# Optimization experiments

Measured on AMD Instinct MI355X. Metric: run time of the kernel, lower is better.

Reference implementation:

```python
import jax, jax.numpy as jnp
import numpy as np

D = 512
SCALE = 1.0 / np.sqrt(D).astype(np.float32)


def setup_inputs() -> dict:
    key = jax.random.key(0)
    ks = jax.random.split(key, 6)
    B, S = 8, 2048
    x = jax.random.normal(ks[0], (B, S, D), dtype=jnp.float32)
    bias = jax.random.normal(ks[1], (1,), dtype=jnp.float32)
    key_padding_mask = jax.random.randint(ks[2], (B, S), 0, 2).astype(jnp.bool_)
    # nn.Linear weights, stored as [out, in]; y = x @ W.T
    Wq = jax.random.normal(ks[3], (D, D), dtype=jnp.float32) * (1.0 / np.sqrt(D))
    Wk = jax.random.normal(ks[4], (D, D), dtype=jnp.float32) * (1.0 / np.sqrt(D))
    Wv = jax.random.normal(ks[5], (D, D), dtype=jnp.float32) * (1.0 / np.sqrt(D))
    return {"x": x, "bias": bias, "key_padding_mask": key_padding_mask,
            "Wq": Wq, "Wk": Wk, "Wv": Wv}


def reference(x, bias, key_padding_mask, Wq, Wk, Wv):
    # Projections (Linear without bias): [B,S,D] @ [D,D]^T
    Q = jnp.einsum('bsd,ed->bse', x, Wq)
    K = jnp.einsum('bsd,ed->bse', x, Wk)
    V = jnp.einsum('bsd,ed->bse', x, Wv)
    # Scaled scores with additive scalar bias: [B,S,S]
    scores = jnp.einsum('bqd,bkd->bqk', Q, K) * SCALE + bias
    # Key padding mask: mask keys (last dim) with -inf
    scores = jnp.where(key_padding_mask[:, None, :], -jnp.inf, scores)
    attn = jax.nn.softmax(scores, axis=-1)
    attn = jnp.nan_to_num(attn, nan=0.0)  # fully-masked rows -> 0
    # Dropout is inference no-op
    return jnp.einsum('bqk,bkd->bqd', attn, V)
```

## Files before the change

kernel.cpp:

```cpp
#include <hip/hip_runtime.h>

typedef short bf16x8 __attribute__((ext_vector_type(8)));
typedef float f32x4 __attribute__((ext_vector_type(4)));
typedef float f32x16 __attribute__((ext_vector_type(16)));
typedef ushort u16x8 __attribute__((ext_vector_type(8)));

__device__ __forceinline__ ushort f2bf(float f) {
    union { float f; unsigned u; } v; v.f = f;
    unsigned r = (v.u + 0x7fffu + ((v.u >> 16) & 1u)) >> 16;
    return (ushort)r;
}
__device__ __forceinline__ float bf2f(ushort u) {
    union { unsigned u; float f; } v; v.u = ((unsigned)u) << 16;
    return v.f;
}
__device__ __forceinline__ void async_copy16(void* lds, const void* g) {
    __builtin_amdgcn_global_load_lds(
        (const __attribute__((address_space(1))) unsigned*)g,
        (__attribute__((address_space(3))) unsigned*)lds, 16, 0, 0);
}

__global__ __launch_bounds__(256)
void prep_kernel(const float* __restrict__ x, const float* __restrict__ Wq,
                 const float* __restrict__ Wk, const float* __restrict__ Wv,
                 const int* __restrict__ mask,
                 ushort* __restrict__ xb, ushort* __restrict__ wqT,
                 ushort* __restrict__ wkT, ushort* __restrict__ wvb,
                 int* __restrict__ idx, int* __restrict__ cnt)
{
    const int bid = blockIdx.x, t = threadIdx.x;
    if (bid < 8192) {
        int i = (bid * 256 + t) * 4;
        float4 v = *(const float4*)(x + i);
        ushort4 o;
        o.x = f2bf(v.x); o.y = f2bf(v.y); o.z = f2bf(v.z); o.w = f2bf(v.w);
        *(ushort4*)(xb + i) = o;
    } else if (bid < 8320) {
        __shared__ ushort T[64][72];
        int r = bid - 8192;
        const int z = r >> 6; r &= 63;
        const float* in = z ? Wk : Wq;
        ushort* out     = z ? wkT : wqT;
        const int r0 = (r >> 3) * 64, c0 = (r & 7) * 64;
        const int rr = t >> 3, cc8 = (t & 7) * 8;
        #pragma unroll
        for (int pass = 0; pass < 2; ++pass) {
            int rw = rr + pass * 32;
            float4 a = *(const float4*)(in + (size_t)(r0 + rw) * 512 + c0 + cc8);
            float4 bq = *(const float4*)(in + (size_t)(r0 + rw) * 512 + c0 + cc8 + 4);
            T[rw][cc8+0]=f2bf(a.x);  T[rw][cc8+1]=f2bf(a.y);  T[rw][cc8+2]=f2bf(a.z);  T[rw][cc8+3]=f2bf(a.w);
            T[rw][cc8+4]=f2bf(bq.x); T[rw][cc8+5]=f2bf(bq.y); T[rw][cc8+6]=f2bf(bq.z); T[rw][cc8+7]=f2bf(bq.w);
        }
        __syncthreads();
        const int c = t >> 2, seg = (t & 3) * 16;
        ushort tmp[16];
        #pragma unroll
        for (int j = 0; j < 16; ++j) tmp[j] = T[seg + j][c];
        *(uint4*)(out + (size_t)(c0 + c) * 512 + r0 + seg)     = *(uint4*)&tmp[0];
        *(uint4*)(out + (size_t)(c0 + c) * 512 + r0 + seg + 8) = *(uint4*)&tmp[8];
    } else if (bid < 8576) {
        int i = ((bid - 8320) * 256 + t) * 4;
        float4 v = *(const float4*)(Wv + i);
        ushort4 o;
        o.x = f2bf(v.x); o.y = f2bf(v.y); o.z = f2bf(v.z); o.w = f2bf(v.w);
        *(ushort4*)(wvb + i) = o;
    } else {
        __shared__ int sc[256];
        int seg = bid - 8576, b = seg >> 1, half = seg & 1;
        const int* m = mask + b * 2048 + half * 1024;
        int v0 = (m[t*4+0] == 0), v1 = (m[t*4+1] == 0);
        int v2 = (m[t*4+2] == 0), v3 = (m[t*4+3] == 0);
        int c = v0 + v1 + v2 + v3;
        sc[t] = c; __syncthreads();
        for (int ofs = 1; ofs < 256; ofs <<= 1) {
            int xx = (t >= ofs) ? sc[t - ofs] : 0;
            __syncthreads(); sc[t] += xx; __syncthreads();
        }
        int pos = sc[t] - c + seg * 1024;
        if (v0) idx[pos++] = t*4+0;
        if (v1) idx[pos++] = t*4+1;
        if (v2) idx[pos++] = t*4+2;
        if (v3) idx[pos++] = t*4+3;
        if (t == 255) cnt[seg] = sc[255];
    }
}

__device__ __forceinline__ int map_row(const int* __restrict__ idx,
                                       const int* __restrict__ cnt, int row) {
    int seg = row >> 10, j = row & 1023;
    int src = (j < cnt[seg]) ? idx[(seg << 10) + j] : 0;
    return (seg << 10) + src;
}

__device__ __forceinline__ void gemm_core(const ushort* __restrict__ A,
                                          const ushort* __restrict__ B,
                                          ushort* __restrict__ C,
                                          int N, int K, int mBase, int nBase,
                                          int mapA, int mapB,
                                          const int* __restrict__ idx,
                                          const int* __restrict__ cnt,
                                          int vt)
{
    __shared__ ushort As[128][32];
    __shared__ ushort Bs[128][32];
    const int tid = threadIdx.x;
    const int lane = tid & 63, wave = tid >> 6;
    const int wm = wave >> 1, wn = wave & 1;
    const int lr = lane & 15, lq = lane >> 4;
    const int sr = lane >> 2;
    const int sc = (lane & 3) * 8;

    const ushort* aptr[2];
    const ushort* bptr[2];
    #pragma unroll
    for (int j = 0; j < 2; ++j) {
        int ra = mBase + wave * 32 + j * 16 + sr;
        int rb = nBase + wave * 32 + j * 16 + sr;
        int sa = mapA ? map_row(idx, cnt, ra) : ra;
        int sb = mapB ? map_row(idx, cnt, rb) : rb;
        aptr[j] = A + (size_t)sa * K + sc;
        bptr[j] = B + (size_t)sb * K + sc;
    }

    f32x4 acc[4][4];
    #pragma unroll
    for (int i = 0; i < 4; ++i)
        #pragma unroll
        for (int j = 0; j < 4; ++j) acc[i][j] = (f32x4){0.f, 0.f, 0.f, 0.f};

    for (int k0 = 0; k0 < K; k0 += 32) {
        __syncthreads();
        #pragma unroll
        for (int j = 0; j < 2; ++j) {
            int rbase = wave * 32 + j * 16;
            async_copy16(&As[rbase][0], aptr[j] + k0);
            async_copy16(&Bs[rbase][0], bptr[j] + k0);
        }
        __syncthreads();
        bf16x8 af[4], bfr[4];
        #pragma unroll
        for (int mi = 0; mi < 4; ++mi) af[mi] = *(const bf16x8*)&As[wm * 64 + mi * 16 + lr][lq * 8];
        #pragma unroll
        for (int ni = 0; ni < 4; ++ni) bfr[ni] = *(const bf16x8*)&Bs[wn * 64 + ni * 16 + lr][lq * 8];
        #pragma unroll
        for (int mi = 0; mi < 4; ++mi)
            #pragma unroll
            for (int ni = 0; ni < 4; ++ni)
                acc[mi][ni] = __builtin_amdgcn_mfma_f32_16x16x32_bf16(af[mi], bfr[ni], acc[mi][ni], 0, 0, 0);
    }
    #pragma unroll
    for (int mi = 0; mi < 4; ++mi)
        #pragma unroll
        for (int ni = 0; ni < 4; ++ni)
            #pragma unroll
            for (int r = 0; r < 4; ++r) {
                int m = mBase + wm * 64 + mi * 16 + lq * 4 + r;
                int n = nBase + wn * 64 + ni * 16 + lr;
                float val = acc[mi][ni][r];
                if (!vt) {
                    C[(size_t)m * N + n] = f2bf(val);
                } else {
                    int sseg = n >> 10, key = n & 1023;
                    int k = key & 15, g2 = (key >> 4) & 1, kt32 = key >> 5;
                    int db = m >> 5, dr = m & 31;
                    size_t ix = (size_t)sseg * 524288 + (size_t)kt32 * 16384
                              + (size_t)(db * 2 + g2) * 512
                              + (size_t)(k >> 3) * 256 + dr * 8 + (k & 7);
                    C[ix] = f2bf(val);
                }
            }
}

__global__ __launch_bounds__(256, 2)
void gemm_m(const ushort* __restrict__ A, const ushort* __restrict__ B,
            ushort* __restrict__ C) {
    gemm_core(A, B, C, 512, 512, blockIdx.y * 128, blockIdx.x * 128,
              0, 0, nullptr, nullptr, 0);
}

__global__ __launch_bounds__(256, 2)
void gemm_kv(const ushort* __restrict__ xb, const ushort* __restrict__ Mb,
             ushort* __restrict__ Kc, const ushort* __restrict__ wv,
             ushort* __restrict__ Vtc, const int* __restrict__ idx,
             const int* __restrict__ cnt)
{
    if (blockIdx.z == 0) {
        int mBase = blockIdx.y * 128, nBase = blockIdx.x * 128;
        if ((mBase & 1023) >= cnt[mBase >> 10]) return;
        gemm_core(xb, Mb, Kc, 512, 512, mBase, nBase, 1, 0, idx, cnt, 0);
    } else {
        int mBase = blockIdx.x * 128, nBase = blockIdx.y * 128;
        if ((nBase & 1023) >= cnt[nBase >> 10]) return;
        gemm_core(wv, xb, Vtc, 16384, 512, mBase, nBase, 0, 1, idx, cnt, 1);
    }
}

__global__ __launch_bounds__(256, 2)
void attn_kernel(const ushort* __restrict__ Qg, const ushort* __restrict__ Kcg,
                 const ushort* __restrict__ Vtcg, const int* __restrict__ cntg,
                 ushort* __restrict__ Pog, float* __restrict__ Mlg)
{
    const int S = 2048;
    const float SL2E = 0.0637587160f;

    __shared__ ushort Ks[32][548];
    __shared__ ushort Vs[16384];
    __shared__ ushort Ps[2][32][36];

    const int lin = blockIdx.x + 32 * blockIdx.y + 256 * blockIdx.z;
    const int seg = (lin & 7) * 2 + (lin >> 8);
    const int qt  = (lin >> 3) & 31;
    const int b = seg >> 1, half = seg & 1;

    const int tid = threadIdx.x, lane = tid & 63, wave = tid >> 6;
    const int lr = lane & 15, lq = lane >> 4;
    const int p = wave >> 1, s = wave & 1;
    const int l32 = lane & 31, lh = lane >> 5;

    const int n = cntg[seg];
    const int ntiles = (n + 31) >> 5;

    const ushort* Qp = Qg + ((size_t)b * S + qt * 64 + wave * 16 + lr) * 512;
    bf16x8 qf[16];
    #pragma unroll
    for (int c = 0; c < 16; ++c) qf[c] = *(const bf16x8*)(Qp + c * 32 + lq * 8);

    f32x16 o[8];
    #pragma unroll
    for (int i = 0; i < 8; ++i)
        #pragma unroll
        for (int r = 0; r < 16; ++r) o[i][r] = 0.f;
    float l_i[4] = {0.f, 0.f, 0.f, 0.f};

    const char* Kseg = (const char*)(Kcg + (size_t)seg * 1024 * 512);
    const char* Vseg = (const char*)(Vtcg + (size_t)seg * 524288);

    {
        #pragma unroll
        for (int i = 0; i < 8; ++i) {
            int row = wave * 8 + i;
            async_copy16(&Ks[row][0], Kseg + (size_t)row * 1024 + lane * 16);
        }
    }

    for (int kt = 0; kt < ntiles; ++kt) {
        const int key0 = kt * 32;
        __syncthreads();
        {
            const char* gV = Vseg + (size_t)kt * 32768;
            #pragma unroll
            for (int i = 0; i < 8; ++i) {
                int chunk = i * 4 + wave;
                async_copy16((char*)Vs + chunk * 1024, gV + chunk * 1024 + lane * 16);
            }
        }
        const bool va0 = (key0 + lr) < n;
        const bool va1 = (key0 + 16 + lr) < n;
        f32x4 sA = (f32x4){0.f,0.f,0.f,0.f}, sB = (f32x4){0.f,0.f,0.f,0.f};
        f32x4 sC = (f32x4){0.f,0.f,0.f,0.f}, sD = (f32x4){0.f,0.f,0.f,0.f};
        __builtin_amdgcn_s_setprio(1);
        #pragma unroll
        for (int ks = 0; ks < 16; ks += 2) {
            bf16x8 kf0a = *(const bf16x8*)&Ks[lr][ks * 32 + lq * 8];
            bf16x8 kf1a = *(const bf16x8*)&Ks[16 + lr][ks * 32 + lq * 8];
            bf16x8 kf0b = *(const bf16x8*)&Ks[lr][(ks + 1) * 32 + lq * 8];
            bf16x8 kf1b = *(const bf16x8*)&Ks[16 + lr][(ks + 1) * 32 + lq * 8];
            sA = __builtin_amdgcn_mfma_f32_16x16x32_bf16(qf[ks], kf0a, sA, 0, 0, 0);
            sB = __builtin_amdgcn_mfma_f32_16x16x32_bf16(qf[ks], kf1a, sB, 0, 0, 0);
            sC = __builtin_amdgcn_mfma_f32_16x16x32_bf16(qf[ks + 1], kf0b, sC, 0, 0, 0);
            sD = __builtin_amdgcn_mfma_f32_16x16x32_bf16(qf[ks + 1], kf1b, sD, 0, 0, 0);
        }
        __builtin_amdgcn_s_setprio(0);
        #pragma unroll
        for (int r = 0; r < 4; ++r) {
            float s0 = sA[r] + sC[r], s1 = sB[r] + sD[r];
            float p0 = va0 ? exp2f(fmaf(s0, SL2E, -8.f)) : 0.f;
            float p1 = va1 ? exp2f(fmaf(s1, SL2E, -8.f)) : 0.f;
            l_i[r] += p0 + p1;
            Ps[p][16 * s + lq * 4 + r][lr]      = f2bf(p0);
            Ps[p][16 * s + lq * 4 + r][16 + lr] = f2bf(p1);
        }
        __syncthreads();
        if (kt + 1 < ntiles) {
            const char* gK = Kseg + (size_t)(key0 + 32) * 1024;
            #pragma unroll
            for (int i = 0; i < 8; ++i) {
                int row = wave * 8 + i;
                async_copy16(&Ks[row][0], gK + (size_t)row * 1024 + lane * 16);
            }
        }
        bf16x8 pA0 = *(const bf16x8*)&Ps[p][l32][lh * 8];
        bf16x8 pA1 = *(const bf16x8*)&Ps[p][l32][16 + lh * 8];
        __builtin_amdgcn_s_setprio(1);
        #pragma unroll
        for (int dt = 0; dt < 8; ++dt) {
            const int db = s * 8 + dt;
            bf16x8 v0 = *(const bf16x8*)((const char*)Vs + (db * 2 + 0) * 1024 + lane * 16);
            bf16x8 v1 = *(const bf16x8*)((const char*)Vs + (db * 2 + 1) * 1024 + lane * 16);
            o[dt] = __builtin_amdgcn_mfma_f32_32x32x16_bf16(pA0, v0, o[dt], 0, 0, 0);
            o[dt] = __builtin_amdgcn_mfma_f32_32x32x16_bf16(pA1, v1, o[dt], 0, 0, 0);
        }
        __builtin_amdgcn_s_setprio(0);
    }
    #pragma unroll
    for (int r = 0; r < 4; ++r)
        #pragma unroll
        for (int off = 1; off < 16; off <<= 1)
            l_i[r] += __shfl_xor(l_i[r], off, 16);
    const size_t growbase = (size_t)half * 16384 + (size_t)b * S + qt * 64;
    if (lr == 0) {
        #pragma unroll
        for (int r = 0; r < 4; ++r)
            Mlg[growbase + wave * 16 + lq * 4 + r] = l_i[r];
    }
    ushort* Pop = Pog + (growbase + p * 32) * 512;
    #pragma unroll
    for (int dt = 0; dt < 8; ++dt) {
        int ocol = s * 256 + dt * 32 + l32;
        #pragma unroll
        for (int r = 0; r < 16; ++r) {
            int orow = (r & 3) + 8 * (r >> 2) + 4 * lh;
            Pop[(size_t)orow * 512 + ocol] = f2bf(o[dt][r]);
        }
    }
}

__global__ __launch_bounds__(256)
void combine_kernel(const ushort* __restrict__ Po, const float* __restrict__ Ml,
                    float* __restrict__ out)
{
    int i = (blockIdx.x * 256 + threadIdx.x) * 8;
    int row = i >> 9;
    float l = Ml[row] + Ml[16384 + row];
    float s = l > 0.f ? 1.f / l : 0.f;
    u16x8 p1 = *(const u16x8*)(Po + i);
    u16x8 p2 = *(const u16x8*)(Po + 8388608 + i);
    float4 o1, o2;
    o1.x = (bf2f((ushort)p1[0]) + bf2f((ushort)p2[0])) * s;
    o1.y = (bf2f((ushort)p1[1]) + bf2f((ushort)p2[1])) * s;
    o1.z = (bf2f((ushort)p1[2]) + bf2f((ushort)p2[2])) * s;
    o1.w = (bf2f((ushort)p1[3]) + bf2f((ushort)p2[3])) * s;
    o2.x = (bf2f((ushort)p1[4]) + bf2f((ushort)p2[4])) * s;
    o2.y = (bf2f((ushort)p1[5]) + bf2f((ushort)p2[5])) * s;
    o2.z = (bf2f((ushort)p1[6]) + bf2f((ushort)p2[6])) * s;
    o2.w = (bf2f((ushort)p1[7]) + bf2f((ushort)p2[7])) * s;
    *(float4*)(out + i)     = o1;
    *(float4*)(out + i + 4) = o2;
}

extern "C" void kernel_launch(void* const* d_in, const int* in_sizes, int n_in,
                              void* d_out, int out_size, void* d_ws, size_t ws_size,
                              hipStream_t stream) {
    const float* x  = (const float*)d_in[0];
    const int* mask = (const int*)d_in[2];
    const float* Wq = (const float*)d_in[3];
    const float* Wk = (const float*)d_in[4];
    const float* Wv = (const float*)d_in[5];
    float* out = (float*)d_out;

    ushort* ws   = (ushort*)d_ws;
    ushort* xb   = ws;
    ushort* wqT  = ws + 8388608;
    ushort* wkT  = wqT + 262144;
    ushort* wvb  = wkT + 262144;
    ushort* Pob  = ws + 9175040;
    ushort* Mb   = ws + 17563648;
    int*    idxb = (int*)(ws + 17825792);
    ushort* Kc   = ws + 25952256;
    ushort* Vtc  = ws + 34340864;
    float*  Mlb  = (float*)(ws + 42729472);
    int*    cntb = (int*)(ws + 42795008);

    prep_kernel<<<8592, 256, 0, stream>>>(x, Wq, Wk, Wv, mask,
                                          xb, wqT, wkT, wvb, idxb, cntb);
    gemm_m<<<dim3(4, 4), 256, 0, stream>>>(wqT, wkT, Mb);
    gemm_kv<<<dim3(4, 128, 2), 256, 0, stream>>>(xb, Mb, Kc, wvb, Vtc, idxb, cntb);
    attn_kernel<<<dim3(32, 8, 2), 256, 0, stream>>>(xb, Kc, Vtc, cntb, Pob, Mlb);
    combine_kernel<<<4096, 256, 0, stream>>>(Pob, Mlb, out);
}
```

Baseline: 198.9 us.

## Fuse Wq^T·Wk product GEMM into prep kernel, drop transpose and separate launch

The small M = Wq^T·Wk GEMM is computed directly inside prep_kernel by 64 blocks that load fp32 weights, convert them to bf16 in LDS in transposed order and run MFMA. This removes the separate gemm_m launch and the intermediate transposed bf16 weight buffers. The trade-off is a less tuned GEMM with small tiles running alongside the conversion blocks, which could become the long pole of the prep kernel.

```diff
diff --git a/kernel.cpp b/kernel.cpp
--- a/kernel.cpp
+++ b/kernel.cpp
@@ -24,49 +24,77 @@
 void prep_kernel(const float* __restrict__ x, const float* __restrict__ Wq,
                  const float* __restrict__ Wk, const float* __restrict__ Wv,
                  const int* __restrict__ mask,
-                 ushort* __restrict__ xb, ushort* __restrict__ wqT,
-                 ushort* __restrict__ wkT, ushort* __restrict__ wvb,
+                 ushort* __restrict__ xb, ushort* __restrict__ wvb,
+                 ushort* __restrict__ Mb,
                  int* __restrict__ idx, int* __restrict__ cnt)
 {
     const int bid = blockIdx.x, t = threadIdx.x;
-    if (bid < 8192) {
-        int i = (bid * 256 + t) * 4;
+    if (bid < 64) {
+        __shared__ ushort As[64][32];
+        __shared__ ushort Bs[64][32];
+        const int m0 = (bid >> 3) * 64, n0 = (bid & 7) * 64;
+        const int lane = t & 63, wave = t >> 6;
+        const int wm = wave >> 1, wn = wave & 1;
+        const int lr = lane & 15, lq = lane >> 4;
+        const int kk = t >> 3, mm = (t & 7) * 8;
+
+        f32x4 acc[2][2];
+        #pragma unroll
+        for (int i2 = 0; i2 < 2; ++i2)
+            #pragma unroll
+            for (int j2 = 0; j2 < 2; ++j2) acc[i2][j2] = (f32x4){0.f,0.f,0.f,0.f};
+
+        for (int k0 = 0; k0 < 512; k0 += 32) {
+            float4 qa0 = *(const float4*)(Wq + (size_t)(k0 + kk) * 512 + m0 + mm);
+            float4 qa1 = *(const float4*)(Wq + (size_t)(k0 + kk) * 512 + m0 + mm + 4);
+            float4 kb0 = *(const float4*)(Wk + (size_t)(k0 + kk) * 512 + n0 + mm);
+            float4 kb1 = *(const float4*)(Wk + (size_t)(k0 + kk) * 512 + n0 + mm + 4);
+            __syncthreads();
+            As[mm + 0][kk] = f2bf(qa0.x); As[mm + 1][kk] = f2bf(qa0.y);
+            As[mm + 2][kk] = f2bf(qa0.z); As[mm + 3][kk] = f2bf(qa0.w);
+            As[mm + 4][kk] = f2bf(qa1.x); As[mm + 5][kk] = f2bf(qa1.y);
+            As[mm + 6][kk] = f2bf(qa1.z); As[mm + 7][kk] = f2bf(qa1.w);
+            Bs[mm + 0][kk] = f2bf(kb0.x); Bs[mm + 1][kk] = f2bf(kb0.y);
+            Bs[mm + 2][kk] = f2bf(kb0.z); Bs[mm + 3][kk] = f2bf(kb0.w);
+            Bs[mm + 4][kk] = f2bf(kb1.x); Bs[mm + 5][kk] = f2bf(kb1.y);
+            Bs[mm + 6][kk] = f2bf(kb1.z); Bs[mm + 7][kk] = f2bf(kb1.w);
+            __syncthreads();
+            bf16x8 af[2], bfr[2];
+            #pragma unroll
+            for (int mi = 0; mi < 2; ++mi) af[mi]  = *(const bf16x8*)&As[wm * 32 + mi * 16 + lr][lq * 8];
+            #pragma unroll
+            for (int ni = 0; ni < 2; ++ni) bfr[ni] = *(const bf16x8*)&Bs[wn * 32 + ni * 16 + lr][lq * 8];
+            #pragma unroll
+            for (int mi = 0; mi < 2; ++mi)
+                #pragma unroll
+                for (int ni = 0; ni < 2; ++ni)
+                    acc[mi][ni] = __builtin_amdgcn_mfma_f32_16x16x32_bf16(af[mi], bfr[ni], acc[mi][ni], 0, 0, 0);
+        }
+        #pragma unroll
+        for (int mi = 0; mi < 2; ++mi)
+            #pragma unroll
+            for (int ni = 0; ni < 2; ++ni)
+                #pragma unroll
+                for (int r = 0; r < 4; ++r) {
+                    int m = m0 + wm * 32 + mi * 16 + lq * 4 + r;
+                    int n = n0 + wn * 32 + ni * 16 + lr;
+                    Mb[(size_t)m * 512 + n] = f2bf(acc[mi][ni][r]);
+                }
+    } else if (bid < 8256) {
+        int i = ((bid - 64) * 256 + t) * 4;
         float4 v = *(const float4*)(x + i);
         ushort4 o;
         o.x = f2bf(v.x); o.y = f2bf(v.y); o.z = f2bf(v.z); o.w = f2bf(v.w);
         *(ushort4*)(xb + i) = o;
-    } else if (bid < 8320) {
-        __shared__ ushort T[64][72];
-        int r = bid - 8192;
-        const int z = r >> 6; r &= 63;
-        const float* in = z ? Wk : Wq;
-        ushort* out     = z ? wkT : wqT;
-        const int r0 = (r >> 3) * 64, c0 = (r & 7) * 64;
-        const int rr = t >> 3, cc8 = (t & 7) * 8;
-        #pragma unroll
-        for (int pass = 0; pass < 2; ++pass) {
-            int rw = rr + pass * 32;
-            float4 a = *(const float4*)(in + (size_t)(r0 + rw) * 512 + c0 + cc8);
-            float4 bq = *(const float4*)(in + (size_t)(r0 + rw) * 512 + c0 + cc8 + 4);
-            T[rw][cc8+0]=f2bf(a.x);  T[rw][cc8+1]=f2bf(a.y);  T[rw][cc8+2]=f2bf(a.z);  T[rw][cc8+3]=f2bf(a.w);
-            T[rw][cc8+4]=f2bf(bq.x); T[rw][cc8+5]=f2bf(bq.y); T[rw][cc8+6]=f2bf(bq.z); T[rw][cc8+7]=f2bf(bq.w);
-        }
-        __syncthreads();
-        const int c = t >> 2, seg = (t & 3) * 16;
-        ushort tmp[16];
-        #pragma unroll
-        for (int j = 0; j < 16; ++j) tmp[j] = T[seg + j][c];
-        *(uint4*)(out + (size_t)(c0 + c) * 512 + r0 + seg)     = *(uint4*)&tmp[0];
-        *(uint4*)(out + (size_t)(c0 + c) * 512 + r0 + seg + 8) = *(uint4*)&tmp[8];
-    } else if (bid < 8576) {
-        int i = ((bid - 8320) * 256 + t) * 4;
+    } else if (bid < 8512) {
+        int i = ((bid - 8256) * 256 + t) * 4;
         float4 v = *(const float4*)(Wv + i);
         ushort4 o;
         o.x = f2bf(v.x); o.y = f2bf(v.y); o.z = f2bf(v.z); o.w = f2bf(v.w);
         *(ushort4*)(wvb + i) = o;
     } else {
         __shared__ int sc[256];
-        int seg = bid - 8576, b = seg >> 1, half = seg & 1;
+        int seg = bid - 8512, b = seg >> 1, half = seg & 1;
         const int* m = mask + b * 2048 + half * 1024;
         int v0 = (m[t*4+0] == 0), v1 = (m[t*4+1] == 0);
         int v2 = (m[t*4+2] == 0), v3 = (m[t*4+3] == 0);
@@ -169,13 +197,6 @@
                     C[ix] = f2bf(val);
                 }
             }
-}
-
-__global__ __launch_bounds__(256, 2)
-void gemm_m(const ushort* __restrict__ A, const ushort* __restrict__ B,
-            ushort* __restrict__ C) {
-    gemm_core(A, B, C, 512, 512, blockIdx.y * 128, blockIdx.x * 128,
-              0, 0, nullptr, nullptr, 0);
 }
 
 __global__ __launch_bounds__(256, 2)
@@ -360,9 +381,7 @@
 
     ushort* ws   = (ushort*)d_ws;
     ushort* xb   = ws;
-    ushort* wqT  = ws + 8388608;
-    ushort* wkT  = wqT + 262144;
-    ushort* wvb  = wkT + 262144;
+    ushort* wvb  = ws + 8912896;
     ushort* Pob  = ws + 9175040;
     ushort* Mb   = ws + 17563648;
     int*    idxb = (int*)(ws + 17825792);
@@ -371,9 +390,8 @@
     float*  Mlb  = (float*)(ws + 42729472);
     int*    cntb = (int*)(ws + 42795008);
 
-    prep_kernel<<<8592, 256, 0, stream>>>(x, Wq, Wk, Wv, mask,
-                                          xb, wqT, wkT, wvb, idxb, cntb);
-    gemm_m<<<dim3(4, 4), 256, 0, stream>>>(wqT, wkT, Mb);
+    prep_kernel<<<8528, 256, 0, stream>>>(x, Wq, Wk, Wv, mask,
+                                          xb, wvb, Mb, idxb, cntb);
     gemm_kv<<<dim3(4, 128, 2), 256, 0, stream>>>(xb, Mb, Kc, wvb, Vtc, idxb, cntb);
     attn_kernel<<<dim3(32, 8, 2), 256, 0, stream>>>(xb, Kc, Vtc, cntb, Pob, Mlb);
     combine_kernel<<<4096, 256, 0, stream>>>(Pob, Mlb, out);
```

After: 197.8 us. Within noise of the previous version (-0.6%).
